# Kernel tuning notes

Measured on AMD Instinct MI355X. Metric: run time of the kernel, lower is better.

The kernel has to match this reference:

```python
import jax, jax.numpy as jnp
import numpy as np

D = 768      # input_dim
O = 768      # output_dim
E = 8        # num_experts
H = 10 * D   # expert hidden dim (fixed by module: input_dim * 10)
N = 4096     # tokens


def setup_inputs() -> dict:
    key = jax.random.key(0)
    ks = jax.random.split(key, 7)
    s = lambda fan_in: 1.0 / np.sqrt(fan_in)
    x  = jax.random.normal(ks[0], (N, D), dtype=jnp.float32)
    Wg = jax.random.uniform(ks[1], (D, E), jnp.float32, -s(D), s(D))
    bg = jax.random.uniform(ks[2], (E,),   jnp.float32, -s(D), s(D))
    W1 = jax.random.uniform(ks[3], (E, D, H), jnp.float32, -s(D), s(D))
    b1 = jax.random.uniform(ks[4], (E, H),    jnp.float32, -s(D), s(D))
    W2 = jax.random.uniform(ks[5], (E, H, O), jnp.float32, -s(H), s(H))
    b2 = jax.random.uniform(ks[6], (E, O),    jnp.float32, -s(H), s(H))
    return {"x": x, "Wg": Wg, "bg": bg, "W1": W1, "b1": b1, "W2": W2, "b2": b2}


def reference(x, Wg, bg, W1, b1, W2, b2):
    # gating: softmax over experts, keep only top-1 prob (rest zeroed)
    gate_probs = jax.nn.softmax(x @ Wg + bg, axis=1)          # [N, E]
    top_vals, top_idx = jax.lax.top_k(gate_probs, 1)           # [N, 1]
    gate_masked = jnp.zeros_like(gate_probs).at[
        jnp.arange(x.shape[0]), top_idx[:, 0]].set(top_vals[:, 0])
    # dense all-experts MLP (module computes every expert for every token)
    h = jax.nn.relu(jnp.einsum('nd,edh->neh', x, W1) + b1)     # [N, E, H]
    expert_out = jnp.einsum('neh,eho->neo', h, W2) + b2        # [N, E, O]
    # bmm combine: [N,1,E] @ [N,E,O] -> [N,O]
    return jnp.einsum('ne,neo->no', gate_masked, expert_out)
```

## Files before the change

### kernel.cpp

```cpp
#include <hip/hip_runtime.h>
#include <hip/hip_bf16.h>
#include <stdint.h>

#define N_TOK 4096
#define DIM   768
#define NE    8
#define HDIM  7680
#define ODIM  768
#define G1GRID 2816
#define G2GRID 1344

typedef __bf16 bf16x8 __attribute__((ext_vector_type(8)));
typedef float f32x4 __attribute__((ext_vector_type(4)));

__device__ __forceinline__ unsigned short f2bf(float f) {
    union { float f; unsigned u; } v; v.f = f;
    return (unsigned short)((v.u + 0x7fffu + ((v.u >> 16) & 1u)) >> 16);
}

__device__ __forceinline__ unsigned cvt_pk_bf16(float lo, float hi) {
    unsigned r;
    asm("v_cvt_pk_bf16_f32 %0, %1, %2" : "=v"(r) : "v"(lo), "v"(hi));
    return r;
}

__device__ __forceinline__ void gload_lds16(const unsigned short* g, unsigned short* l) {
    __builtin_amdgcn_global_load_lds(
        (const __attribute__((address_space(1))) unsigned int*)g,
        (__attribute__((address_space(3))) unsigned int*)l, 16, 0, 0);
}

__global__ void moe_gating(const float* __restrict__ x, const float* __restrict__ Wg,
                           const float* __restrict__ bg, int* __restrict__ cnt,
                           int* __restrict__ top_e, int* __restrict__ rnk,
                           float* __restrict__ top_p) {
    const int wid  = threadIdx.x >> 6;
    const int lane = threadIdx.x & 63;
    const int t = blockIdx.x * 4 + wid;
    double p[NE];
#pragma unroll
    for (int j = 0; j < NE; ++j) p[j] = 0.0;
    const float* xr  = x  + (size_t)t * DIM + lane * 12;
    const float* wr0 = Wg + lane * 12 * NE;
#pragma unroll
    for (int i = 0; i < 12; ++i) {
        double xv = (double)xr[i];
#pragma unroll
        for (int j = 0; j < NE; ++j) p[j] += xv * (double)wr0[i * NE + j];
    }
#pragma unroll
    for (int off = 32; off >= 1; off >>= 1)
#pragma unroll
        for (int j = 0; j < NE; ++j) p[j] += __shfl_xor(p[j], off, 64);
    if (lane == 0) {
        double l[NE];
#pragma unroll
        for (int j = 0; j < NE; ++j) l[j] = p[j] + (double)bg[j];
        int be = 0; double bl = l[0];
#pragma unroll
        for (int j = 1; j < NE; ++j) if (l[j] > bl) { bl = l[j]; be = j; }
        double s = 0.0;
#pragma unroll
        for (int j = 0; j < NE; ++j) s += exp(l[j] - bl);
        int rk = atomicAdd(&cnt[be], 1);
        top_e[t] = be; rnk[t] = rk; top_p[t] = (float)(1.0 / s);
    }
}

__global__ void moe_init(int* cnt) { if (threadIdx.x < NE) cnt[threadIdx.x] = 0; }

__global__ void moe_scan(const int* __restrict__ cnt, int* __restrict__ offs,
                         int* __restrict__ mc, int* __restrict__ g1s,
                         int* __restrict__ g2s) {
    __shared__ int smc[NE];
    int tid = threadIdx.x;
    if (tid == 0) { int s = 0; for (int e = 0; e < NE; ++e) { offs[e] = s; s += cnt[e]; } }
    if (tid < NE) { smc[tid] = (cnt[tid] + 127) >> 7; mc[tid] = smc[tid]; }
    __syncthreads();
    if (tid < 8) {
        int s = 0;
        for (int j = 0; j < 60; ++j) { int p = tid + 8 * j; g1s[p] = s; s += smc[p / 60]; }
        int s2 = 0;
        for (int j = 0; j < 6; ++j)  { int p = tid + 8 * j; g2s[p] = s2; s2 += 4 * smc[p / 6]; }
    }
}

__global__ void moe_fill(const int* __restrict__ mc, const int* __restrict__ g1s,
                         const int* __restrict__ g2s, int* __restrict__ tbl1,
                         int* __restrict__ tbl2) {
    int gid = blockIdx.x * 256 + threadIdx.x;
    if (gid < G1GRID) {
        int c = gid & 7, slot = gid >> 3;
        int sel = c;
        for (int j = 0; j < 60; ++j) { int p = c + 8 * j; if (g1s[p] <= slot) sel = p; else break; }
        int e = sel / 60, n0 = sel % 60;
        int mt = slot - g1s[sel];
        tbl1[gid] = (mt < mc[e]) ? ((e << 14) | (mt << 8) | (n0 << 2)) : -1;
    } else if (gid < G1GRID + G2GRID) {
        int gg = gid - G1GRID;
        int c = gg & 7, slot = gg >> 3;
        int sel = c;
        for (int j = 0; j < 6; ++j) { int p = c + 8 * j; if (g2s[p] <= slot) sel = p; else break; }
        int e = sel / 6, n0 = sel % 6;
        int mem = slot - g2s[sel];
        int mcE = mc[e];
        int ks = mem / mcE, mt = mem - ks * mcE;
        tbl2[gg] = (mem < 4 * mcE) ? ((e << 14) | (mt << 8) | (n0 << 2) | ks) : -1;
    }
}

__global__ void moe_mkperm(const int* __restrict__ top_e, const int* __restrict__ rnk,
                           const float* __restrict__ top_p, const int* __restrict__ offs,
                           int* __restrict__ perm, float* __restrict__ gate_s) {
    int t = blockIdx.x * 256 + threadIdx.x;
    int e = top_e[t];
    int slot = offs[e] + rnk[t];
    perm[slot] = t;
    gate_s[slot] = top_p[t];
}

__global__ void moe_gather(const float* __restrict__ x, const int* __restrict__ perm,
                           unsigned short* __restrict__ Xg) {
    int slot = blockIdx.x;
    int t = perm[slot];
    const float* src = x + (size_t)t * DIM;
    unsigned short* dst = Xg + (size_t)slot * DIM;
    for (int i = threadIdx.x; i < DIM; i += 256) dst[i] = f2bf(src[i]);
}

__global__ void moe_initout(const int* __restrict__ top_e, const float* __restrict__ top_p,
                            const float* __restrict__ b2, float* __restrict__ out) {
    int t = blockIdx.x;
    int e = top_e[t];
    float gv = top_p[t];
    const float* b = b2 + (size_t)e * ODIM;
    float* o = out + (size_t)t * ODIM;
    for (int i = threadIdx.x; i < ODIM; i += 256) o[i] = gv * b[i];
}

template<int LAYER>
__global__ __launch_bounds__(256, 3) void moe_gemm(
    const unsigned short* __restrict__ A, const float* __restrict__ B,
    const float* __restrict__ bias, const int* __restrict__ cnt,
    const int* __restrict__ offs, const int* __restrict__ perm,
    const float* __restrict__ gate_s, const int* __restrict__ tbl,
    unsigned short* __restrict__ H, float* __restrict__ out) {

    constexpr int NT    = (LAYER == 1) ? HDIM : ODIM;
    constexpr int AST   = (LAYER == 1) ? DIM  : HDIM;
    constexpr int KFULL = (LAYER == 1) ? DIM  : HDIM;
    constexpr int KBLK  = (LAYER == 1) ? DIM  : HDIM / 4;
    constexpr int NITER = KBLK / 32;

    const int code = tbl[blockIdx.x];
    if (code < 0) return;
    const int e  = code >> 14;
    const int mt = (code >> 8) & 63;
    const int n0 = ((code >> 2) & 63) * 128;
    const int ks = code & 3;
    const int ne = cnt[e];
    const int base = offs[e];
    const int mlim = ne - mt * 128;
    const int kbase = ks * KBLK;

    __shared__ unsigned short As[3][4096];
    __shared__ unsigned short Bs[2][4096];

    const int tid = threadIdx.x;
    const int lane = tid & 63, w = tid >> 6;
    const int wr = w >> 1, wc = w & 1;
    const int g = lane >> 4, r = lane & 15;

    const int rl0 = 2 * w * 16 + r;
    const int rl1 = rl0 + 16;
    const int cr0 = rl0 < mlim ? rl0 : mlim - 1;
    const int cr1 = rl1 < mlim ? rl1 : mlim - 1;
    const unsigned short* aS0 = A + (size_t)(base + mt * 128 + cr0) * AST + kbase + g * 8;
    const unsigned short* aS1 = A + (size_t)(base + mt * 128 + cr1) * AST + kbase + g * 8;
    const int aD0 = (2 * w) * 512;
    const int aD1 = aD0 + 512;

    const int bn = tid & 127;
    const int kh = tid >> 7;
    const float* bS = B + (size_t)e * KFULL * NT + (size_t)(kbase + kh * 16) * NT + n0 + bn;
    const int bD = (bn >> 4) * 512 + (kh * 2) * 128 + (bn & 15) * 8;

    f32x4 acc[4][4] = {};
    float bvA[16], bvB[16];

    unsigned short* A0 = &As[0][0];
    unsigned short* A1 = &As[1][0];
    unsigned short* A2 = &As[2][0];

#define FENCE __builtin_amdgcn_sched_barrier(0)

#define LOADB(dst_, t_)                                                        \
    do { const float* bp_ = bS + (size_t)((t_) * 32) * NT;                     \
        _Pragma("unroll")                                                      \
        for (int i_ = 0; i_ < 16; ++i_) dst_[i_] = bp_[(size_t)i_ * NT];       \
    } while (0)

#define DMA_A(t_, abase_)                                                      \
    do { gload_lds16(aS0 + (t_) * 32, (abase_) + aD0);                         \
         gload_lds16(aS1 + (t_) * 32, (abase_) + aD1); } while (0)

#define COMMITB(src_, buf_)                                                    \
    do { uint4 q0_, q1_;                                                       \
        q0_.x = cvt_pk_bf16(src_[0],  src_[1]);  q0_.y = cvt_pk_bf16(src_[2],  src_[3]);  \
        q0_.z = cvt_pk_bf16(src_[4],  src_[5]);  q0_.w = cvt_pk_bf16(src_[6],  src_[7]);  \
        q1_.x = cvt_pk_bf16(src_[8],  src_[9]);  q1_.y = cvt_pk_bf16(src_[10], src_[11]); \
        q1_.z = cvt_pk_bf16(src_[12], src_[13]); q1_.w = cvt_pk_bf16(src_[14], src_[15]); \
        *(uint4*)&Bs[buf_][bD]       = q0_;                                    \
        *(uint4*)&Bs[buf_][bD + 128] = q1_;                                    \
    } while (0)

#define BODY(t_, cur_, ARD_, ADMA_, LDst_, CMsrc_, MODE_)                      \
    do {                                                                       \
        bf16x8 af_[4], bf_[4];                                                 \
        _Pragma("unroll")                                                      \
        for (int m_ = 0; m_ < 4; ++m_)                                         \
            af_[m_] = *(const bf16x8*)((ARD_) + (wr * 4 + m_) * 512 + lane * 8); \
        _Pragma("unroll")                                                      \
        for (int n_ = 0; n_ < 4; ++n_)                                         \
            bf_[n_] = *(const bf16x8*)&Bs[cur_][(wc * 4 + n_) * 512 + lane * 8]; \
        FENCE;                                                                 \
        if (MODE_ == 2) DMA_A((t_) + 2, ADMA_);                                \
        FENCE;                                                                 \
        if (MODE_ == 2) LOADB(LDst_, (t_) + 2);                                \
        asm volatile("s_waitcnt lgkmcnt(0)" ::: "memory");                     \
        FENCE;                                                                 \
        _Pragma("unroll")                                                      \
        for (int n_ = 0; n_ < 4; ++n_)                                         \
            _Pragma("unroll")                                                  \
            for (int m_ = 0; m_ < 4; ++m_)                                     \
                acc[m_][n_] = __builtin_amdgcn_mfma_f32_16x16x32_bf16(         \
                    af_[m_], bf_[n_], acc[m_][n_], 0, 0, 0);                   \
        FENCE;                                                                 \
        if (MODE_ == 2) { asm volatile("s_waitcnt vmcnt(18)" ::: "memory"); }  \
        else if (MODE_ == 1) { asm volatile("s_waitcnt vmcnt(0)" ::: "memory"); } \
        if (MODE_ >= 1) {                                                      \
            COMMITB(CMsrc_, (cur_) ^ 1);                                       \
            asm volatile("s_waitcnt lgkmcnt(0)" ::: "memory");                 \
            __builtin_amdgcn_s_barrier();                                      \
            FENCE;                                                             \
        }                                                                      \
    } while (0)

    DMA_A(0, A0);
    FENCE;
    LOADB(bvA, 0);
    FENCE;
    DMA_A(1, A1);
    FENCE;
    LOADB(bvB, 1);
    asm volatile("s_waitcnt vmcnt(18)" ::: "memory");
    FENCE;
    COMMITB(bvA, 0);
    asm volatile("s_waitcnt lgkmcnt(0)" ::: "memory");
    __builtin_amdgcn_s_barrier();
    FENCE;

#pragma unroll 1
    for (int t = 0; t + 4 <= NITER; t += 2) {
        BODY(t,     0, A0, A2, bvA, bvB, 2);
        BODY(t + 1, 1, A1, A0, bvB, bvA, 2);
        unsigned short* tr_ = A2; A2 = A1; A1 = A0; A0 = tr_;
    }
    BODY(NITER - 2, 0, A0, A2, bvA, bvB, 1);
    BODY(NITER - 1, 1, A1, A2, bvB, bvA, 0);

#undef BODY
#undef COMMITB
#undef DMA_A
#undef LOADB
#undef FENCE

#pragma unroll
    for (int m = 0; m < 4; ++m) {
#pragma unroll
        for (int j = 0; j < 4; ++j) {
            int lrow = mt * 128 + wr * 64 + m * 16 + g * 4 + j;
            if (lrow < ne) {
                int slot = base + lrow;
#pragma unroll
                for (int n = 0; n < 4; ++n) {
                    int col = n0 + wc * 64 + n * 16 + r;
                    if constexpr (LAYER == 1) {
                        float v = acc[m][n][j] + bias[(size_t)e * NT + col];
                        v = fmaxf(v, 0.0f);
                        H[(size_t)slot * HDIM + col] = f2bf(v);
                    } else {
                        atomicAdd(&out[(size_t)perm[slot] * ODIM + col],
                                  gate_s[slot] * acc[m][n][j]);
                    }
                }
            }
        }
    }
}

extern "C" void kernel_launch(void* const* d_in, const int* in_sizes, int n_in,
                              void* d_out, int out_size, void* d_ws, size_t ws_size,
                              hipStream_t stream) {
    const float* x  = (const float*)d_in[0];
    const float* Wg = (const float*)d_in[1];
    const float* bg = (const float*)d_in[2];
    const float* W1 = (const float*)d_in[3];
    const float* b1 = (const float*)d_in[4];
    const float* W2 = (const float*)d_in[5];
    const float* b2 = (const float*)d_in[6];
    float* out = (float*)d_out;

    char* ws = (char*)d_ws;
    int*   cnt    = (int*)(ws + 0);
    int*   offs   = (int*)(ws + 64);
    int*   mc     = (int*)(ws + 128);
    int*   g1s    = (int*)(ws + 256);
    int*   g2s    = (int*)(ws + 2304);
    int*   tbl1   = (int*)(ws + 3072);
    int*   tbl2   = (int*)(ws + 14336);
    int*   top_e  = (int*)(ws + 19712);
    int*   rnk    = (int*)(ws + 19712 + 16384);
    float* top_p  = (float*)(ws + 19712 + 2 * 16384);
    int*   perm   = (int*)(ws + 19712 + 3 * 16384);
    float* gate_s = (float*)(ws + 19712 + 4 * 16384);
    unsigned short* Xg = (unsigned short*)(ws + 101632);
    unsigned short* H  = (unsigned short*)(ws + 101632 + (size_t)N_TOK * DIM * 2);

    moe_init<<<1, 64, 0, stream>>>(cnt);
    moe_gating<<<N_TOK / 4, 256, 0, stream>>>(x, Wg, bg, cnt, top_e, rnk, top_p);
    moe_scan<<<1, 64, 0, stream>>>(cnt, offs, mc, g1s, g2s);
    moe_fill<<<(G1GRID + G2GRID + 255) / 256, 256, 0, stream>>>(mc, g1s, g2s, tbl1, tbl2);
    moe_mkperm<<<N_TOK / 256, 256, 0, stream>>>(top_e, rnk, top_p, offs, perm, gate_s);
    moe_gather<<<N_TOK, 256, 0, stream>>>(x, perm, Xg);
    moe_initout<<<N_TOK, 256, 0, stream>>>(top_e, top_p, b2, out);

    moe_gemm<1><<<G1GRID, 256, 0, stream>>>(Xg, W1, b1, cnt, offs, perm, gate_s, tbl1, H, out);
    moe_gemm<2><<<G2GRID, 256, 0, stream>>>(H, W2, b2, cnt, offs, perm, gate_s, tbl2, H, out);
}
```

Measured before the change: 367.8 us.

## Pre-transpose expert weights to bf16 and DMA B tiles directly into LDS

Result: slower. 459.6 us (+25.0%).

```diff
diff --git a/kernel.cpp b/kernel.cpp
--- a/kernel.cpp
+++ b/kernel.cpp
@@ -9,6 +9,7 @@
 #define ODIM  768
 #define G1GRID 2816
 #define G2GRID 1344
+#define WS_NEED 258051328ull
 
 typedef __bf16 bf16x8 __attribute__((ext_vector_type(8)));
 typedef float f32x4 __attribute__((ext_vector_type(4)));
@@ -138,13 +139,43 @@
     for (int i = threadIdx.x; i < ODIM; i += 256) o[i] = gv * b[i];
 }
 
-template<int LAYER>
+__global__ __launch_bounds__(256) void moe_wtrans(const float* __restrict__ in,
+                                                  unsigned short* __restrict__ outw,
+                                                  int K, int N) {
+    __shared__ __align__(16) unsigned short t[64][72];
+    const int tid = threadIdx.x;
+    const float* src = in + (size_t)blockIdx.z * K * N + (size_t)(blockIdx.y * 64) * N
+                          + blockIdx.x * 64;
+    unsigned short* dst = outw + (size_t)blockIdx.z * K * N + (size_t)(blockIdx.x * 64) * K
+                               + blockIdx.y * 64;
+    const int kr = tid >> 4;
+    const int nc = (tid & 15) * 4;
+#pragma unroll
+    for (int p = 0; p < 4; ++p) {
+        float4 v = *(const float4*)(src + (size_t)(p * 16 + kr) * N + nc);
+        t[nc + 0][p * 16 + kr] = f2bf(v.x);
+        t[nc + 1][p * 16 + kr] = f2bf(v.y);
+        t[nc + 2][p * 16 + kr] = f2bf(v.z);
+        t[nc + 3][p * 16 + kr] = f2bf(v.w);
+    }
+    __syncthreads();
+    const int nr = tid >> 3;
+    const int kc = (tid & 7) * 8;
+#pragma unroll
+    for (int p = 0; p < 2; ++p) {
+        uint4 q = *(const uint4*)&t[p * 32 + nr][kc];
+        *(uint4*)(dst + (size_t)(p * 32 + nr) * K + kc) = q;
+    }
+}
+
+template<int LAYER, bool TB>
 __global__ __launch_bounds__(256, 3) void moe_gemm(
-    const unsigned short* __restrict__ A, const float* __restrict__ B,
-    const float* __restrict__ bias, const int* __restrict__ cnt,
-    const int* __restrict__ offs, const int* __restrict__ perm,
-    const float* __restrict__ gate_s, const int* __restrict__ tbl,
-    unsigned short* __restrict__ H, float* __restrict__ out) {
+    const unsigned short* __restrict__ A, const float* __restrict__ Bf,
+    const unsigned short* __restrict__ Bt, const float* __restrict__ bias,
+    const int* __restrict__ cnt, const int* __restrict__ offs,
+    const int* __restrict__ perm, const float* __restrict__ gate_s,
+    const int* __restrict__ tbl, unsigned short* __restrict__ H,
+    float* __restrict__ out) {
 
     constexpr int NT    = (LAYER == 1) ? HDIM : ODIM;
     constexpr int AST   = (LAYER == 1) ? DIM  : HDIM;
@@ -163,8 +194,8 @@
     const int mlim = ne - mt * 128;
     const int kbase = ks * KBLK;
 
-    __shared__ unsigned short As[3][4096];
-    __shared__ unsigned short Bs[2][4096];
+    __shared__ __align__(16) unsigned short As[3][4096];
+    __shared__ __align__(16) unsigned short Bs[TB ? 3 : 2][4096];
 
     const int tid = threadIdx.x;
     const int lane = tid & 63, w = tid >> 6;
@@ -180,30 +211,81 @@
     const int aD0 = (2 * w) * 512;
     const int aD1 = aD0 + 512;
 
-    const int bn = tid & 127;
-    const int kh = tid >> 7;
-    const float* bS = B + (size_t)e * KFULL * NT + (size_t)(kbase + kh * 16) * NT + n0 + bn;
-    const int bD = (bn >> 4) * 512 + (kh * 2) * 128 + (bn & 15) * 8;
-
     f32x4 acc[4][4] = {};
-    float bvA[16], bvB[16];
-
-    unsigned short* A0 = &As[0][0];
-    unsigned short* A1 = &As[1][0];
-    unsigned short* A2 = &As[2][0];
 
 #define FENCE __builtin_amdgcn_sched_barrier(0)
-
-#define LOADB(dst_, t_)                                                        \
-    do { const float* bp_ = bS + (size_t)((t_) * 32) * NT;                     \
-        _Pragma("unroll")                                                      \
-        for (int i_ = 0; i_ < 16; ++i_) dst_[i_] = bp_[(size_t)i_ * NT];       \
-    } while (0)
-
 #define DMA_A(t_, abase_)                                                      \
     do { gload_lds16(aS0 + (t_) * 32, (abase_) + aD0);                         \
          gload_lds16(aS1 + (t_) * 32, (abase_) + aD1); } while (0)
 
+    if constexpr (TB) {
+        const unsigned short* Be = Bt + (size_t)e * KFULL * NT;
+        const unsigned short* bS0 = Be + (size_t)(n0 + rl0) * KFULL + kbase + g * 8;
+        const unsigned short* bS1 = Be + (size_t)(n0 + rl1) * KFULL + kbase + g * 8;
+
+        unsigned short* A0 = &As[0][0]; unsigned short* A1 = &As[1][0]; unsigned short* A2 = &As[2][0];
+        unsigned short* B0 = &Bs[0][0]; unsigned short* B1 = &Bs[1][0]; unsigned short* B2 = &Bs[2][0];
+
+#define DMA_B(t_, bbase_)                                                      \
+    do { gload_lds16(bS0 + (t_) * 32, (bbase_) + aD0);                         \
+         gload_lds16(bS1 + (t_) * 32, (bbase_) + aD1); } while (0)
+
+#define BODYW(t_, ARD_, BRD_, ADMA_, BDMA_, MODE_)                             \
+    do {                                                                       \
+        bf16x8 af_[4], bf_[4];                                                 \
+        _Pragma("unroll")                                                      \
+        for (int m_ = 0; m_ < 4; ++m_)                                         \
+            af_[m_] = *(const bf16x8*)((ARD_) + (wr * 4 + m_) * 512 + lane * 8); \
+        _Pragma("unroll")                                                      \
+        for (int n_ = 0; n_ < 4; ++n_)                                         \
+            bf_[n_] = *(const bf16x8*)((BRD_) + (wc * 4 + n_) * 512 + lane * 8); \
+        FENCE;                                                                 \
+        if (MODE_ == 2) { DMA_A((t_) + 2, ADMA_); DMA_B((t_) + 2, BDMA_); }    \
+        asm volatile("s_waitcnt lgkmcnt(0)" ::: "memory");                     \
+        FENCE;                                                                 \
+        _Pragma("unroll")                                                      \
+        for (int n_ = 0; n_ < 4; ++n_)                                         \
+            _Pragma("unroll")                                                  \
+            for (int m_ = 0; m_ < 4; ++m_)                                     \
+                acc[m_][n_] = __builtin_amdgcn_mfma_f32_16x16x32_bf16(         \
+                    af_[m_], bf_[n_], acc[m_][n_], 0, 0, 0);                   \
+        FENCE;                                                                 \
+        if (MODE_ == 2) { asm volatile("s_waitcnt vmcnt(4)" ::: "memory"); }   \
+        else if (MODE_ == 1) { asm volatile("s_waitcnt vmcnt(0)" ::: "memory"); } \
+        if (MODE_ >= 1) { __builtin_amdgcn_s_barrier(); FENCE; }               \
+    } while (0)
+
+        DMA_A(0, A0); DMA_B(0, B0);
+        FENCE;
+        DMA_A(1, A1); DMA_B(1, B1);
+        asm volatile("s_waitcnt vmcnt(4)" ::: "memory");
+        __builtin_amdgcn_s_barrier();
+        FENCE;
+
+#pragma unroll 1
+        for (int t = 0; t + 4 <= NITER; t += 2) {
+            BODYW(t,     A0, B0, A2, B2, 2);
+            BODYW(t + 1, A1, B1, A0, B0, 2);
+            unsigned short* ta_ = A2; A2 = A1; A1 = A0; A0 = ta_;
+            unsigned short* tb_ = B2; B2 = B1; B1 = B0; B0 = tb_;
+        }
+        BODYW(NITER - 2, A0, B0, A2, B2, 1);
+        BODYW(NITER - 1, A1, B1, A2, B2, 0);
+#undef BODYW
+#undef DMA_B
+    } else {
+        const int bn = tid & 127;
+        const int kh = tid >> 7;
+        const float* bS = Bf + (size_t)e * KFULL * NT + (size_t)(kbase + kh * 16) * NT + n0 + bn;
+        const int bD = (bn >> 4) * 512 + (kh * 2) * 128 + (bn & 15) * 8;
+        float bvA[16], bvB[16];
+        unsigned short* A0 = &As[0][0]; unsigned short* A1 = &As[1][0]; unsigned short* A2 = &As[2][0];
+
+#define LOADB(dst_, t_)                                                        \
+    do { const float* bp_ = bS + (size_t)((t_) * 32) * NT;                     \
+        _Pragma("unroll")                                                      \
+        for (int i_ = 0; i_ < 16; ++i_) dst_[i_] = bp_[(size_t)i_ * NT];       \
+    } while (0)
 #define COMMITB(src_, buf_)                                                    \
     do { uint4 q0_, q1_;                                                       \
         q0_.x = cvt_pk_bf16(src_[0],  src_[1]);  q0_.y = cvt_pk_bf16(src_[2],  src_[3]);  \
@@ -213,8 +295,7 @@
         *(uint4*)&Bs[buf_][bD]       = q0_;                                    \
         *(uint4*)&Bs[buf_][bD + 128] = q1_;                                    \
     } while (0)
-
-#define BODY(t_, cur_, ARD_, ADMA_, LDst_, CMsrc_, MODE_)                      \
+#define BODYR(t_, cur_, ARD_, ADMA_, LDst_, CMsrc_, MODE_)                     \
     do {                                                                       \
         bf16x8 af_[4], bf_[4];                                                 \
         _Pragma("unroll")                                                      \
@@ -246,33 +327,33 @@
         }                                                                      \
     } while (0)
 
-    DMA_A(0, A0);
-    FENCE;
-    LOADB(bvA, 0);
-    FENCE;
-    DMA_A(1, A1);
-    FENCE;
-    LOADB(bvB, 1);
-    asm volatile("s_waitcnt vmcnt(18)" ::: "memory");
-    FENCE;
-    COMMITB(bvA, 0);
-    asm volatile("s_waitcnt lgkmcnt(0)" ::: "memory");
-    __builtin_amdgcn_s_barrier();
-    FENCE;
+        DMA_A(0, A0);
+        FENCE;
+        LOADB(bvA, 0);
+        FENCE;
+        DMA_A(1, A1);
+        FENCE;
+        LOADB(bvB, 1);
+        asm volatile("s_waitcnt vmcnt(18)" ::: "memory");
+        FENCE;
+        COMMITB(bvA, 0);
+        asm volatile("s_waitcnt lgkmcnt(0)" ::: "memory");
+        __builtin_amdgcn_s_barrier();
+        FENCE;
 
 #pragma unroll 1
-    for (int t = 0; t + 4 <= NITER; t += 2) {
-        BODY(t,     0, A0, A2, bvA, bvB, 2);
-        BODY(t + 1, 1, A1, A0, bvB, bvA, 2);
-        unsigned short* tr_ = A2; A2 = A1; A1 = A0; A0 = tr_;
-    }
-    BODY(NITER - 2, 0, A0, A2, bvA, bvB, 1);
-    BODY(NITER - 1, 1, A1, A2, bvB, bvA, 0);
-
-#undef BODY
+        for (int t = 0; t + 4 <= NITER; t += 2) {
+            BODYR(t,     0, A0, A2, bvA, bvB, 2);
+            BODYR(t + 1, 1, A1, A0, bvB, bvA, 2);
+            unsigned short* tr_ = A2; A2 = A1; A1 = A0; A0 = tr_;
+        }
+        BODYR(NITER - 2, 0, A0, A2, bvA, bvB, 1);
+        BODYR(NITER - 1, 1, A1, A2, bvB, bvA, 0);
+#undef BODYR
 #undef COMMITB
+#undef LOADB
+    }
 #undef DMA_A
-#undef LOADB
 #undef FENCE
 
 #pragma unroll
@@ -324,8 +405,11 @@
     float* top_p  = (float*)(ws + 19712 + 2 * 16384);
     int*   perm   = (int*)(ws + 19712 + 3 * 16384);
     float* gate_s = (float*)(ws + 19712 + 4 * 16384);
-    unsigned short* Xg = (unsigned short*)(ws + 101632);
-    unsigned short* H  = (unsigned short*)(ws + 101632 + (size_t)N_TOK * DIM * 2);
+    unsigned short* Xg  = (unsigned short*)(ws + 101632);
+    unsigned short* H   = (unsigned short*)(ws + 101632 + (size_t)N_TOK * DIM * 2);
+    unsigned short* W1t = (unsigned short*)(ws + 69307648ull);
+    unsigned short* W2t = (unsigned short*)(ws + 163679488ull);
+    const bool big = (ws_size >= WS_NEED);
 
     moe_init<<<1, 64, 0, stream>>>(cnt);
     moe_gating<<<N_TOK / 4, 256, 0, stream>>>(x, Wg, bg, cnt, top_e, rnk, top_p);
@@ -335,6 +419,17 @@
     moe_gather<<<N_TOK, 256, 0, stream>>>(x, perm, Xg);
     moe_initout<<<N_TOK, 256, 0, stream>>>(top_e, top_p, b2, out);
 
-    moe_gemm<1><<<G1GRID, 256, 0, stream>>>(Xg, W1, b1, cnt, offs, perm, gate_s, tbl1, H, out);
-    moe_gemm<2><<<G2GRID, 256, 0, stream>>>(H, W2, b2, cnt, offs, perm, gate_s, tbl2, H, out);
-}
+    if (big) {
+        moe_wtrans<<<dim3(HDIM / 64, DIM / 64, NE), 256, 0, stream>>>(W1, W1t, DIM, HDIM);
+        moe_wtrans<<<dim3(ODIM / 64, HDIM / 64, NE), 256, 0, stream>>>(W2, W2t, HDIM, ODIM);
+        moe_gemm<1, true><<<G1GRID, 256, 0, stream>>>(
+            Xg, W1, W1t, b1, cnt, offs, perm, gate_s, tbl1, H, out);
+        moe_gemm<2, true><<<G2GRID, 256, 0, stream>>>(
+            H, W2, W2t, b2, cnt, offs, perm, gate_s, tbl2, H, out);
+    } else {
+        moe_gemm<1, false><<<G1GRID, 256, 0, stream>>>(
+            Xg, W1, W1t, b1, cnt, offs, perm, gate_s, tbl1, H, out);
+        moe_gemm<2, false><<<G2GRID, 256, 0, stream>>>(
+            H, W2, W2t, b2, cnt, offs, perm, gate_s, tbl2, H, out);
+    }
+}
```
